# Kernel optimization log

Measured on AMD Instinct MI355X. Metric: run time of the kernel, lower is better.

The kernel has to match this reference:

```python
import jax, jax.numpy as jnp
import numpy as np
from jax import lax

# Kernel / geometry constants matching init_kwargs
KZ, KX, KY = 9, 15, 15          # PSF support
STRIDE = (1, 1, 1)              # scale = (zscale, xscale, yscale)
Z_PAD = (KZ - 1 + 1) // 2       # 4
X_PAD = (KX - 1 + 1) // 2       # 7
Y_PAD = (KY - 1 + 1) // 2       # 7


def _dist(n):
    # |idx - n//2|, matching _distance_from_center
    return jnp.abs(jnp.arange(n, dtype=jnp.float32) - n // 2)


def gen_psf(bet_xy, bet_z, alpha):
    b = bet_xy.shape[0]
    zd = _dist(KZ)                                  # [KZ]
    xd = _dist(KX)
    yd = _dist(KY)
    # gen_distance_plane: dp[i, j] = xd[j]^2 + yd[i]^2  (shape [KY, KX])
    dp = yd[:, None] ** 2 + xd[None, :] ** 2
    # gen_2dnorm: [b, KY, KX]
    bxy = bet_xy[:, None, None]
    lat = jnp.exp(-dp[None] / (2.0 * bxy ** 2)) / (2.0 * jnp.pi * bxy ** 2)
    # gen_1dnorm: [b, KZ]
    bz = bet_z[:, None]
    ax = jnp.exp(-(zd[None] ** 2) / (2.0 * bz ** 2)) / (jnp.sqrt(2.0 * jnp.pi) * bz)
    # psf = exp(log(lateral) + log(axial)) == lateral * axial  -> [b, 1, KZ, KY, KX]
    psf = lat[:, None, None, :, :] * ax[:, None, :, None, None]
    # double_exp mode
    psf = 1.0 - jnp.exp(-alpha[:, None, None, None, None] * psf)
    return psf / jnp.sum(psf)


def reference(x, bet_xy, bet_z, alpha):
    # x: [B, 1, Z, X, Y]; original computes dense conv3d giving [B, B, ...] and
    # keeps only the diagonal _x[b, b]. That is mathematically a per-sample
    # (grouped) convolution, implemented here without the O(B) redundancy.
    psf = gen_psf(bet_xy, bet_z, alpha)             # [B, 1, KZ, KY, KX]
    B = x.shape[0]
    xin = jnp.transpose(x, (1, 0, 2, 3, 4))         # [1, B, Z, X, Y]
    out = lax.conv_general_dilated(
        xin, psf,
        window_strides=STRIDE,
        padding=[(Z_PAD, Z_PAD), (X_PAD, X_PAD), (Y_PAD, Y_PAD)],
        dimension_numbers=("NCDHW", "OIDHW", "NCDHW"),
        feature_group_count=B,
    )                                               # [1, B, Z', X', Y']
    return jnp.transpose(out, (1, 0, 2, 3, 4))      # [B, 1, Z', X', Y']


def setup_inputs() -> dict:
    key = jax.random.key(0)
    k1, k2, k3, k4 = jax.random.split(key, 4)
    B = 4
    x = jax.random.normal(k1, (B, 1, 32, 192, 192), dtype=jnp.float32)
    bet_xy = 1.0 + 2.0 * jax.random.uniform(k2, (B,), dtype=jnp.float32)   # in [1, 3)
    bet_z = 1.0 + 2.0 * jax.random.uniform(k3, (B,), dtype=jnp.float32)    # in [1, 3)
    alpha = 1.0 + 9.0 * jax.random.uniform(k4, (B,), dtype=jnp.float32)    # in [1, 10)
    return {"x": x, "bet_xy": bet_xy, "bet_z": bet_z, "alpha": alpha}
```

## Files before the change

kernel.cpp:

```cpp
#include <hip/hip_runtime.h>
#include <math.h>

#define B_ 4
#define D_ 32
#define H_ 192
#define W_ 192
#define HW_ (H_ * W_)

#define NT 5

#define TW 48
#define TH 12
#define NTHR 192
#define ZCHUNK 16
#define NP (ZCHUNK + 8)

#define XT_H 26
#define XT_W 64
#define XT_SZ (XT_H * XT_W)
#define XT_Q (XT_H * 16)

#define SMEM_WORDS (2 * XT_SZ)

#define NTAPS (B_ * 9 * 15 * 15)
#define WS_FLOATS (B_ * 65)

__device__ inline float4 f4fma(float c, float4 a, float4 d) {
    d.x = fmaf(c, a.x, d.x); d.y = fmaf(c, a.y, d.y);
    d.z = fmaf(c, a.z, d.z); d.w = fmaf(c, a.w, d.w);
    return d;
}
__device__ inline float4 f4add(float4 a, float4 b) {
    a.x += b.x; a.y += b.y; a.z += b.z; a.w += b.w; return a;
}
__device__ inline float rfl(float x) {
    return __int_as_float(__builtin_amdgcn_readfirstlane(__float_as_int(x)));
}
template<int N>
__device__ inline float dpp_shl(float v) {
    return __int_as_float(__builtin_amdgcn_update_dpp(
        0, __float_as_int(v), 0x100 | N, 0xF, 0xF, true));
}
template<int N>
__device__ inline float dpp_shr(float v) {
    return __int_as_float(__builtin_amdgcn_update_dpp(
        0, __float_as_int(v), 0x110 | N, 0xF, 0xF, true));
}

__device__ inline float tap_val(int idx, const float* bet_xy,
                                const float* bet_z, const float* alpha) {
    const float INV = 0.3989422804014327f;
    int bb = idx / 2025;
    int r  = idx % 2025;
    int dz = r / 225;
    int r2 = r % 225;
    int dh = r2 / 15;
    int dw = r2 % 15;
    float bxy = bet_xy[bb], bzv = bet_z[bb], al = alpha[bb];
    float zd = (float)(dz - 4), hd = (float)(dh - 7), wd = (float)(dw - 7);
    float az = expf(-zd * zd / (2.f * bzv * bzv)) * (INV / bzv);
    float gh = expf(-hd * hd / (2.f * bxy * bxy)) * (INV / bxy);
    float gw = expf(-wd * wd / (2.f * bxy * bxy)) * (INV / bxy);
    return 1.f - expf(-al * az * gh * gw);
}

__device__ inline float ct_val(int bb, int n, int k, float S,
                               const float* bet_xy, const float* bet_z,
                               const float* alpha) {
    const float INV = 0.3989422804014327f;
    float bxy = bet_xy[bb], bzv = bet_z[bb], al = alpha[bb];
    if (k < 8) {
        float d = (float)k;
        float g = expf(-d * d / (2.f * bxy * bxy)) * (INV / bxy);
        float p = g;
        for (int q = 0; q < n; ++q) p *= g;
        return p;
    } else {
        float d = (float)(k - 8);
        float az = expf(-d * d / (2.f * bzv * bzv)) * (INV / bzv);
        float base = al * az;
        float p = base;
        for (int q = 0; q < n; ++q) p *= base;
        const float facs[NT] = {1.f, 2.f, 6.f, 24.f, 120.f};
        float sign = (n & 1) ? -1.f : 1.f;
        return sign * p / (facs[n] * S);
    }
}

__global__ __launch_bounds__(256)
void psf_precompute(const float* __restrict__ bet_xy,
                    const float* __restrict__ bet_z,
                    const float* __restrict__ alpha,
                    float* __restrict__ ws) {
    __shared__ float red[256];
    const int t = threadIdx.x;
    float local = 0.f;
#pragma unroll
    for (int s = 0; s < 32; ++s) {
        int idx = t + s * 256;
        if (idx < NTAPS) local += tap_val(idx, bet_xy, bet_z, alpha);
    }
    red[t] = local;
    __syncthreads();
    for (int s = 128; s > 0; s >>= 1) {
        if (t < s) red[t] += red[t + s];
        __syncthreads();
    }
    const float S = red[0];
    if (t < WS_FLOATS) {
        int bb = t / 65, j = t % 65;
        ws[t] = ct_val(bb, j / 13, j % 13, S, bet_xy, bet_z, alpha);
    }
}

template<bool USE_WS>
__global__ __launch_bounds__(NTHR)
void conv_kernel(const float* __restrict__ x,
                 const float* __restrict__ bet_xy,
                 const float* __restrict__ bet_z,
                 const float* __restrict__ alpha,
                 const float* __restrict__ ct_ws,
                 float* __restrict__ out) {
    __shared__ __align__(16) float smem[SMEM_WORDS];
    float* xtb = smem;
    float* red = smem;
    float* ct  = smem;

    const int t  = threadIdx.x;
    const int w0 = blockIdx.x * TW;
    const int h0 = blockIdx.y * TH;
    const int bz = blockIdx.z;
    const int b  = bz & 3;
    const int z0 = (bz >> 2) * ZCHUNK;
    const float4 z4 = make_float4(0.f, 0.f, 0.f, 0.f);

    if (USE_WS) {
        if (t < 65) ct[t] = ct_ws[b * 65 + t];
        __syncthreads();
    } else {
        float local = 0.f;
#pragma unroll
        for (int s = 0; s < 43; ++s) {
            int idx = t + s * NTHR;
            if (idx < NTAPS) local += tap_val(idx, bet_xy, bet_z, alpha);
        }
        red[t] = local;
        __syncthreads();
        for (int s = 128; s > 0; s >>= 1) {
            if (t < s && t + s < NTHR) red[t] += red[t + s];
            __syncthreads();
        }
        const float S = red[0];
        __syncthreads();
        if (t < 65) ct[t] = ct_val(b, t / 13, t % 13, S, bet_xy, bet_z, alpha);
        __syncthreads();
    }

    float cg_[NT][8], cz_[NT][5];
#pragma unroll
    for (int n = 0; n < NT; ++n) {
#pragma unroll
        for (int k = 0; k < 8; ++k) cg_[n][k] = rfl(ct[n * 13 + k]);
#pragma unroll
        for (int k = 0; k < 5; ++k) cz_[n][k] = rfl(ct[n * 13 + 8 + k]);
    }
    __syncthreads();

    const float* xb = x + (size_t)b * (D_ * HW_);
    int goff[3];
#pragma unroll
    for (int k = 0; k < 3; ++k) {
        int i = t + NTHR * k;
        if (i < XT_Q) {
            int row = i >> 4, qq = i & 15;
            int gh = h0 + row - 7, gc = w0 - 8 + 4 * qq;
            bool ok = (gh >= 0) && (gh < H_) && (gc >= 0) && (gc <= W_ - 4);
            goff[k] = ok ? (gh * W_ + gc) : -1;
        } else {
            goff[k] = -2;
        }
    }
    {
        int zi0 = z0 - 4;
        if (zi0 >= 0) {
            const float* xp = xb + (size_t)zi0 * HW_;
            float4* xn = (float4*)xtb;
            xn[t]        = (goff[0] >= 0) ? *(const float4*)(xp + goff[0]) : z4;
            xn[t + 192]  = (goff[1] >= 0) ? *(const float4*)(xp + goff[1]) : z4;
            if (goff[2] != -2)
                xn[t + 384] = (goff[2] >= 0) ? *(const float4*)(xp + goff[2]) : z4;
        }
    }

    const int r1 = t >> 4;
    const int q  = t & 15;
    const bool qreal = (q >= 2) && (q <= 13);

    float4 acc[9];
#pragma unroll
    for (int k = 0; k < 9; ++k) acc[k] = z4;

#pragma unroll 1
    for (int p = 0; p < NP; ++p) {
        __syncthreads();

        const int zi = z0 - 4 + p;
        const bool do_c = (zi >= 0) && (zi < D_);
        const int  zn = zi + 1;
        const bool pvalid = (p + 1 < NP) && (zn >= 0) && (zn < D_);

        float4 pv0, pv1, pv2;
        if (pvalid) {
            const float* xp = xb + (size_t)zn * HW_;
            pv0 = (goff[0] >= 0) ? *(const float4*)(xp + goff[0]) : z4;
            pv1 = (goff[1] >= 0) ? *(const float4*)(xp + goff[1]) : z4;
            pv2 = z4;
            if (goff[2] >= 0) pv2 = *(const float4*)(xp + goff[2]);
        }

        if (do_c) {
            const float4* x4 = (const float4*)(xtb + (p & 1) * XT_SZ) + t;
            float4 ctr = x4[7 * 16];
            float4 sp[7];
#pragma unroll
            for (int k = 1; k <= 7; ++k)
                sp[k - 1] = f4add(x4[(7 - k) * 16], x4[(7 + k) * 16]);
            float4 u[5];
#pragma unroll
            for (int n = 0; n < NT; ++n) {
                float c0 = cg_[n][0];
                float4 hr;
                hr.x = c0 * ctr.x; hr.y = c0 * ctr.y;
                hr.z = c0 * ctr.z; hr.w = c0 * ctr.w;
#pragma unroll
                for (int k = 1; k <= 7; ++k) hr = f4fma(cg_[n][k], sp[k - 1], hr);
                float win[20];
                win[8]  = hr.x; win[9]  = hr.y; win[10] = hr.z; win[11] = hr.w;
                win[0]  = dpp_shr<2>(hr.x); win[1]  = dpp_shr<2>(hr.y);
                win[2]  = dpp_shr<2>(hr.z); win[3]  = dpp_shr<2>(hr.w);
                win[4]  = dpp_shr<1>(hr.x); win[5]  = dpp_shr<1>(hr.y);
                win[6]  = dpp_shr<1>(hr.z); win[7]  = dpp_shr<1>(hr.w);
                win[12] = dpp_shl<1>(hr.x); win[13] = dpp_shl<1>(hr.y);
                win[14] = dpp_shl<1>(hr.z); win[15] = dpp_shl<1>(hr.w);
                win[16] = dpp_shl<2>(hr.x); win[17] = dpp_shl<2>(hr.y);
                win[18] = dpp_shl<2>(hr.z); win[19] = dpp_shl<2>(hr.w);
                float4 qv;
                qv.x = c0 * win[8];  qv.y = c0 * win[9];
                qv.z = c0 * win[10]; qv.w = c0 * win[11];
#pragma unroll
                for (int k = 1; k <= 7; ++k) {
                    float c = cg_[n][k];
                    qv.x = fmaf(c, win[8 - k]  + win[8 + k],  qv.x);
                    qv.y = fmaf(c, win[9 - k]  + win[9 + k],  qv.y);
                    qv.z = fmaf(c, win[10 - k] + win[10 + k], qv.z);
                    qv.w = fmaf(c, win[11 - k] + win[11 + k], qv.w);
                }
                if (n == 0) {
#pragma unroll
                    for (int j = 0; j < 5; ++j) {
                        float cz = cz_[0][j];
                        u[j].x = cz * qv.x; u[j].y = cz * qv.y;
                        u[j].z = cz * qv.z; u[j].w = cz * qv.w;
                    }
                } else {
#pragma unroll
                    for (int j = 0; j < 5; ++j)
                        u[j] = f4fma(cz_[n][j], qv, u[j]);
                }
            }
            acc[4] = f4add(acc[4], u[0]);
#pragma unroll
            for (int j = 1; j <= 4; ++j) {
                acc[4 + j] = f4add(acc[4 + j], u[j]);
                acc[4 - j] = f4add(acc[4 - j], u[j]);
            }
        }

        if (p >= 8 && qreal) {
            int z = z0 + (p - 8);
            size_t o = ((size_t)(b * D_ + z) * H_ + (h0 + r1)) * W_ + (w0 - 8 + 4 * q);
            *(float4*)&out[o] = acc[0];
        }
#pragma unroll
        for (int k = 0; k < 8; ++k) acc[k] = acc[k + 1];
        acc[8] = z4;

        if (pvalid) {
            float4* xn = (float4*)(xtb + ((p + 1) & 1) * XT_SZ);
            xn[t]       = pv0;
            xn[t + 192] = pv1;
            if (goff[2] != -2) xn[t + 384] = pv2;
        }
    }
}

extern "C" void kernel_launch(void* const* d_in, const int* in_sizes, int n_in,
                              void* d_out, int out_size, void* d_ws, size_t ws_size,
                              hipStream_t stream) {
    const float* x      = (const float*)d_in[0];
    const float* bet_xy = (const float*)d_in[1];
    const float* bet_z  = (const float*)d_in[2];
    const float* alpha  = (const float*)d_in[3];
    float* out = (float*)d_out;

    dim3 grid(W_ / TW, H_ / TH, B_ * (D_ / ZCHUNK));
    if (d_ws != nullptr && ws_size >= WS_FLOATS * sizeof(float)) {
        hipLaunchKernelGGL(psf_precompute, dim3(1), dim3(256), 0, stream,
                           bet_xy, bet_z, alpha, (float*)d_ws);
        hipLaunchKernelGGL(HIP_KERNEL_NAME(conv_kernel<true>), grid, dim3(NTHR),
                           0, stream, x, bet_xy, bet_z, alpha,
                           (const float*)d_ws, out);
    } else {
        hipLaunchKernelGGL(HIP_KERNEL_NAME(conv_kernel<false>), grid, dim3(NTHR),
                           0, stream, x, bet_xy, bet_z, alpha,
                           (const float*)nullptr, out);
    }
}
```

Baseline: 134.1 us.

## Process two z-planes per barrier with quad-buffered LDS and widen PSF precompute

The conv kernel's main loop now handles two z-planes per iteration. It uses four LDS plane buffers and prefetches the next two planes into registers, which halves the number of __syncthreads and gives more loads in flight per barrier. The PSF normalization precompute moves from 256 to 1024 threads, so each thread evaluates fewer taps serially. The cost is double the shared memory, more live registers for the prefetched values (which may lower occupancy), and a longer reduction tree.

Result: faster. 130.4 us (-2.8%).

```diff
diff --git a/kernel.cpp b/kernel.cpp
--- a/kernel.cpp
+++ b/kernel.cpp
@@ -14,13 +14,14 @@
 #define NTHR 192
 #define ZCHUNK 16
 #define NP (ZCHUNK + 8)
+#define NITER (NP / 2)
 
 #define XT_H 26
 #define XT_W 64
 #define XT_SZ (XT_H * XT_W)
 #define XT_Q (XT_H * 16)
 
-#define SMEM_WORDS (2 * XT_SZ)
+#define SMEM_WORDS (4 * XT_SZ)
 
 #define NTAPS (B_ * 9 * 15 * 15)
 #define WS_FLOATS (B_ * 65)
@@ -87,22 +88,22 @@
     }
 }
 
-__global__ __launch_bounds__(256)
+__global__ __launch_bounds__(1024)
 void psf_precompute(const float* __restrict__ bet_xy,
                     const float* __restrict__ bet_z,
                     const float* __restrict__ alpha,
                     float* __restrict__ ws) {
-    __shared__ float red[256];
+    __shared__ float red[1024];
     const int t = threadIdx.x;
     float local = 0.f;
 #pragma unroll
-    for (int s = 0; s < 32; ++s) {
-        int idx = t + s * 256;
+    for (int s = 0; s < 8; ++s) {
+        int idx = t + s * 1024;
         if (idx < NTAPS) local += tap_val(idx, bet_xy, bet_z, alpha);
     }
     red[t] = local;
     __syncthreads();
-    for (int s = 128; s > 0; s >>= 1) {
+    for (int s = 512; s > 0; s >>= 1) {
         if (t < s) red[t] += red[t + s];
         __syncthreads();
     }
@@ -180,17 +181,18 @@
             goff[k] = -2;
         }
     }
-    {
-        int zi0 = z0 - 4;
-        if (zi0 >= 0) {
-            const float* xp = xb + (size_t)zi0 * HW_;
-            float4* xn = (float4*)xtb;
-            xn[t]        = (goff[0] >= 0) ? *(const float4*)(xp + goff[0]) : z4;
-            xn[t + 192]  = (goff[1] >= 0) ? *(const float4*)(xp + goff[1]) : z4;
+    auto stage = [&](int zi, int bi) {
+        if (zi >= 0 && zi < D_) {
+            const float* xp = xb + (size_t)zi * HW_;
+            float4* xn = (float4*)(xtb + bi * XT_SZ);
+            xn[t]       = (goff[0] >= 0) ? *(const float4*)(xp + goff[0]) : z4;
+            xn[t + 192] = (goff[1] >= 0) ? *(const float4*)(xp + goff[1]) : z4;
             if (goff[2] != -2)
                 xn[t + 384] = (goff[2] >= 0) ? *(const float4*)(xp + goff[2]) : z4;
         }
-    }
+    };
+    stage(z0 - 4, 0);
+    stage(z0 - 3, 1);
 
     const int r1 = t >> 4;
     const int q  = t & 15;
@@ -200,82 +202,65 @@
 #pragma unroll
     for (int k = 0; k < 9; ++k) acc[k] = z4;
 
-#pragma unroll 1
-    for (int p = 0; p < NP; ++p) {
-        __syncthreads();
-
-        const int zi = z0 - 4 + p;
-        const bool do_c = (zi >= 0) && (zi < D_);
-        const int  zn = zi + 1;
-        const bool pvalid = (p + 1 < NP) && (zn >= 0) && (zn < D_);
-
-        float4 pv0, pv1, pv2;
-        if (pvalid) {
-            const float* xp = xb + (size_t)zn * HW_;
-            pv0 = (goff[0] >= 0) ? *(const float4*)(xp + goff[0]) : z4;
-            pv1 = (goff[1] >= 0) ? *(const float4*)(xp + goff[1]) : z4;
-            pv2 = z4;
-            if (goff[2] >= 0) pv2 = *(const float4*)(xp + goff[2]);
-        }
-
-        if (do_c) {
-            const float4* x4 = (const float4*)(xtb + (p & 1) * XT_SZ) + t;
-            float4 ctr = x4[7 * 16];
-            float4 sp[7];
-#pragma unroll
-            for (int k = 1; k <= 7; ++k)
-                sp[k - 1] = f4add(x4[(7 - k) * 16], x4[(7 + k) * 16]);
-            float4 u[5];
-#pragma unroll
-            for (int n = 0; n < NT; ++n) {
-                float c0 = cg_[n][0];
-                float4 hr;
-                hr.x = c0 * ctr.x; hr.y = c0 * ctr.y;
-                hr.z = c0 * ctr.z; hr.w = c0 * ctr.w;
-#pragma unroll
-                for (int k = 1; k <= 7; ++k) hr = f4fma(cg_[n][k], sp[k - 1], hr);
-                float win[20];
-                win[8]  = hr.x; win[9]  = hr.y; win[10] = hr.z; win[11] = hr.w;
-                win[0]  = dpp_shr<2>(hr.x); win[1]  = dpp_shr<2>(hr.y);
-                win[2]  = dpp_shr<2>(hr.z); win[3]  = dpp_shr<2>(hr.w);
-                win[4]  = dpp_shr<1>(hr.x); win[5]  = dpp_shr<1>(hr.y);
-                win[6]  = dpp_shr<1>(hr.z); win[7]  = dpp_shr<1>(hr.w);
-                win[12] = dpp_shl<1>(hr.x); win[13] = dpp_shl<1>(hr.y);
-                win[14] = dpp_shl<1>(hr.z); win[15] = dpp_shl<1>(hr.w);
-                win[16] = dpp_shl<2>(hr.x); win[17] = dpp_shl<2>(hr.y);
-                win[18] = dpp_shl<2>(hr.z); win[19] = dpp_shl<2>(hr.w);
-                float4 qv;
-                qv.x = c0 * win[8];  qv.y = c0 * win[9];
-                qv.z = c0 * win[10]; qv.w = c0 * win[11];
-#pragma unroll
-                for (int k = 1; k <= 7; ++k) {
-                    float c = cg_[n][k];
-                    qv.x = fmaf(c, win[8 - k]  + win[8 + k],  qv.x);
-                    qv.y = fmaf(c, win[9 - k]  + win[9 + k],  qv.y);
-                    qv.z = fmaf(c, win[10 - k] + win[10 + k], qv.z);
-                    qv.w = fmaf(c, win[11 - k] + win[11 + k], qv.w);
+    auto do_plane = [&](int zi, int bi) {
+        if (zi < 0 || zi >= D_) return;
+        const float4* x4 = (const float4*)(xtb + bi * XT_SZ) + t;
+        float4 ctr = x4[7 * 16];
+        float4 sp[7];
+#pragma unroll
+        for (int k = 1; k <= 7; ++k)
+            sp[k - 1] = f4add(x4[(7 - k) * 16], x4[(7 + k) * 16]);
+        float4 u[5];
+#pragma unroll
+        for (int n = 0; n < NT; ++n) {
+            float c0 = cg_[n][0];
+            float4 hr;
+            hr.x = c0 * ctr.x; hr.y = c0 * ctr.y;
+            hr.z = c0 * ctr.z; hr.w = c0 * ctr.w;
+#pragma unroll
+            for (int k = 1; k <= 7; ++k) hr = f4fma(cg_[n][k], sp[k - 1], hr);
+            float win[20];
+            win[8]  = hr.x; win[9]  = hr.y; win[10] = hr.z; win[11] = hr.w;
+            win[0]  = dpp_shr<2>(hr.x); win[1]  = dpp_shr<2>(hr.y);
+            win[2]  = dpp_shr<2>(hr.z); win[3]  = dpp_shr<2>(hr.w);
+            win[4]  = dpp_shr<1>(hr.x); win[5]  = dpp_shr<1>(hr.y);
+            win[6]  = dpp_shr<1>(hr.z); win[7]  = dpp_shr<1>(hr.w);
+            win[12] = dpp_shl<1>(hr.x); win[13] = dpp_shl<1>(hr.y);
+            win[14] = dpp_shl<1>(hr.z); win[15] = dpp_shl<1>(hr.w);
+            win[16] = dpp_shl<2>(hr.x); win[17] = dpp_shl<2>(hr.y);
+            win[18] = dpp_shl<2>(hr.z); win[19] = dpp_shl<2>(hr.w);
+            float4 qv;
+            qv.x = c0 * win[8];  qv.y = c0 * win[9];
+            qv.z = c0 * win[10]; qv.w = c0 * win[11];
+#pragma unroll
+            for (int k = 1; k <= 7; ++k) {
+                float c = cg_[n][k];
+                qv.x = fmaf(c, win[8 - k]  + win[8 + k],  qv.x);
+                qv.y = fmaf(c, win[9 - k]  + win[9 + k],  qv.y);
+                qv.z = fmaf(c, win[10 - k] + win[10 + k], qv.z);
+                qv.w = fmaf(c, win[11 - k] + win[11 + k], qv.w);
+            }
+            if (n == 0) {
+#pragma unroll
+                for (int j = 0; j < 5; ++j) {
+                    float cz = cz_[0][j];
+                    u[j].x = cz * qv.x; u[j].y = cz * qv.y;
+                    u[j].z = cz * qv.z; u[j].w = cz * qv.w;
                 }
-                if (n == 0) {
-#pragma unroll
-                    for (int j = 0; j < 5; ++j) {
-                        float cz = cz_[0][j];
-                        u[j].x = cz * qv.x; u[j].y = cz * qv.y;
-                        u[j].z = cz * qv.z; u[j].w = cz * qv.w;
-                    }
-                } else {
-#pragma unroll
-                    for (int j = 0; j < 5; ++j)
-                        u[j] = f4fma(cz_[n][j], qv, u[j]);
-                }
+            } else {
+#pragma unroll
+                for (int j = 0; j < 5; ++j)
+                    u[j] = f4fma(cz_[n][j], qv, u[j]);
             }
-            acc[4] = f4add(acc[4], u[0]);
-#pragma unroll
-            for (int j = 1; j <= 4; ++j) {
-                acc[4 + j] = f4add(acc[4 + j], u[j]);
-                acc[4 - j] = f4add(acc[4 - j], u[j]);
-            }
-        }
-
+        }
+        acc[4] = f4add(acc[4], u[0]);
+#pragma unroll
+        for (int j = 1; j <= 4; ++j) {
+            acc[4 + j] = f4add(acc[4 + j], u[j]);
+            acc[4 - j] = f4add(acc[4 - j], u[j]);
+        }
+    };
+    auto store_shift = [&](int p) {
         if (p >= 8 && qreal) {
             int z = z0 + (p - 8);
             size_t o = ((size_t)(b * D_ + z) * H_ + (h0 + r1)) * W_ + (w0 - 8 + 4 * q);
@@ -284,12 +269,50 @@
 #pragma unroll
         for (int k = 0; k < 8; ++k) acc[k] = acc[k + 1];
         acc[8] = z4;
-
-        if (pvalid) {
-            float4* xn = (float4*)(xtb + ((p + 1) & 1) * XT_SZ);
-            xn[t]       = pv0;
-            xn[t + 192] = pv1;
-            if (goff[2] != -2) xn[t + 384] = pv2;
+    };
+
+#pragma unroll 1
+    for (int i = 0; i < NITER; ++i) {
+        __syncthreads();
+
+        const int pA = 2 * i;
+        const int ziA = z0 - 4 + pA;
+        const int bA = (i & 1) * 2;
+        const int znC = ziA + 2, znD = ziA + 3;
+        const bool vC = (pA + 2 < NP) && (znC >= 0) && (znC < D_);
+        const bool vD = (pA + 3 < NP) && (znD >= 0) && (znD < D_);
+
+        float4 cv0, cv1, cv2, dv0, dv1, dv2;
+        if (vC) {
+            const float* xp = xb + (size_t)znC * HW_;
+            cv0 = (goff[0] >= 0) ? *(const float4*)(xp + goff[0]) : z4;
+            cv1 = (goff[1] >= 0) ? *(const float4*)(xp + goff[1]) : z4;
+            cv2 = z4;
+            if (goff[2] >= 0) cv2 = *(const float4*)(xp + goff[2]);
+        }
+        if (vD) {
+            const float* xp = xb + (size_t)znD * HW_;
+            dv0 = (goff[0] >= 0) ? *(const float4*)(xp + goff[0]) : z4;
+            dv1 = (goff[1] >= 0) ? *(const float4*)(xp + goff[1]) : z4;
+            dv2 = z4;
+            if (goff[2] >= 0) dv2 = *(const float4*)(xp + goff[2]);
+        }
+
+        do_plane(ziA, bA);
+        store_shift(pA);
+        do_plane(ziA + 1, bA + 1);
+        store_shift(pA + 1);
+
+        const int bC = ((i + 1) & 1) * 2;
+        if (vC) {
+            float4* xn = (float4*)(xtb + bC * XT_SZ);
+            xn[t] = cv0; xn[t + 192] = cv1;
+            if (goff[2] != -2) xn[t + 384] = cv2;
+        }
+        if (vD) {
+            float4* xn = (float4*)(xtb + (bC + 1) * XT_SZ);
+            xn[t] = dv0; xn[t + 192] = dv1;
+            if (goff[2] != -2) xn[t + 384] = dv2;
         }
     }
 }
@@ -305,7 +328,7 @@
 
     dim3 grid(W_ / TW, H_ / TH, B_ * (D_ / ZCHUNK));
     if (d_ws != nullptr && ws_size >= WS_FLOATS * sizeof(float)) {
-        hipLaunchKernelGGL(psf_precompute, dim3(1), dim3(256), 0, stream,
+        hipLaunchKernelGGL(psf_precompute, dim3(1), dim3(1024), 0, stream,
                            bet_xy, bet_z, alpha, (float*)d_ws);
         hipLaunchKernelGGL(HIP_KERNEL_NAME(conv_kernel<true>), grid, dim3(NTHR),
                            0, stream, x, bet_xy, bet_z, alpha,
```
